# Kernel tuning notes

Hardware: AMD Instinct MI355X
Metric: run time of the kernel (lower is better)

The kernel has to match this reference:

```python
import jax, jax.numpy as jnp
import numpy as np

N = 100000
E = 1000000
IN_C, HID, OUT_C = 64, 64, 40


def setup_inputs() -> dict:
    key = jax.random.key(0)
    ks = jax.random.split(key, 12)
    x = jax.random.normal(ks[0], (N, IN_C), dtype=jnp.float32)
    edge_index = jax.random.randint(ks[1], (2, E), 0, N, dtype=jnp.int64)

    def glorot(k, fan_in, fan_out):
        s = (6.0 / (fan_in + fan_out)) ** 0.5
        return jax.random.uniform(k, (fan_in, fan_out), jnp.float32, -s, s)

    return {
        "x": x,
        "edge_index": edge_index,
        "W1": glorot(ks[2], IN_C, HID), "b1": jnp.zeros((HID,), jnp.float32),
        "W2": glorot(ks[3], HID, HID), "b2": jnp.zeros((HID,), jnp.float32),
        "Wm1": glorot(ks[4], HID, HID), "bm1": jnp.zeros((HID,), jnp.float32),
        "Wm2": glorot(ks[5], HID, OUT_C), "bm2": jnp.zeros((OUT_C,), jnp.float32),
    }


def _gcn_conv(h_in, W, b, src, dst, deg_inv_sqrt):
    # PyG GCNConv: x' = D^{-1/2} (A + I) D^{-1/2} (x W) + b, self-loops added.
    h = h_in @ W                                        # [N, F]
    norm = deg_inv_sqrt[src] * deg_inv_sqrt[dst]        # [E]
    msg = h[src] * norm[:, None]                        # gather + scale
    agg = jax.ops.segment_sum(msg, dst, num_segments=N)  # scatter-add
    # self-loop contribution: deg_i^{-1/2} * deg_i^{-1/2} * h_i
    agg = agg + h * (deg_inv_sqrt * deg_inv_sqrt)[:, None]
    return agg + b


def reference(x, edge_index, W1, b1, W2, b2, Wm1, bm1, Wm2, bm2):
    src, dst = edge_index[0], edge_index[1]
    deg = jax.ops.segment_sum(jnp.ones((E,), jnp.float32), dst, num_segments=N) + 1.0
    deg_inv_sqrt = jax.lax.rsqrt(deg)

    h = _gcn_conv(x, W1, b1, src, dst, deg_inv_sqrt)
    h = jax.nn.relu(h)
    h = _gcn_conv(h, W2, b2, src, dst, deg_inv_sqrt)  # no relu after last conv

    h = jax.nn.relu(h @ Wm1 + bm1)
    out = h @ Wm2 + bm2
    return out
```

## Files before the change

kernel.cpp:

```cpp
#include <hip/hip_runtime.h>
#include <hip/hip_bf16.h>
#include <hip/hip_fp16.h>


namespace {

constexpr int N_NODES = 100000;
constexpr int N_EDGES = 1000000;
constexpr int NBUCK = (N_NODES + 511) / 512;
constexpr int CAP_RAW = 8192;
constexpr int CAP_COL = 12288;
constexpr int EPB_A = 2048;

__global__ __launch_bounds__(256) void bucket_kernel(const void* __restrict__ ei,
                                                     int* __restrict__ bucketCnt,
                                                     unsigned* __restrict__ tmp) {
  __shared__ int hist[NBUCK];
  __shared__ int basePB[NBUCK];
  __shared__ int cur[NBUCK];
  __shared__ int sflag;
  int t = threadIdx.x;
  if (t < NBUCK) { hist[t] = 0; cur[t] = 0; }
  if (t == 0) sflag = 0;
  __syncthreads();

  int e0 = blockIdx.x * EPB_A;
  const unsigned* w = (const unsigned*)ei;
  unsigned any = 0;
#pragma unroll
  for (int s = 0; s < 2; s++) {
    int e = e0 + s * 256 + t;
    if (e < N_EDGES) any |= w[2 * e + 1];
  }
  if (any) sflag = 1;
  __syncthreads();
  int is32 = sflag;

  unsigned wreg[8];
  int breg[8];
#pragma unroll
  for (int k = 0; k < 8; k++) {
    int e = e0 + k * 256 + t;
    breg[k] = -1;
    if (e < N_EDGES) {
      int s, d;
      if (is32) {
        const int* p = (const int*)ei;
        s = p[e]; d = p[N_EDGES + e];
      } else {
        const long long* p = (const long long*)ei;
        s = (int)p[e]; d = (int)p[N_EDGES + e];
      }
      wreg[k] = ((unsigned)s << 9) | (unsigned)(d & 511);
      breg[k] = d >> 9;
      atomicAdd(&hist[breg[k]], 1);
    }
  }
  __syncthreads();
  if (t < NBUCK) basePB[t] = hist[t] ? atomicAdd(&bucketCnt[t], hist[t]) : 0;
  __syncthreads();
#pragma unroll
  for (int k = 0; k < 8; k++) {
    if (breg[k] >= 0) {
      int r = atomicAdd(&cur[breg[k]], 1);
      tmp[(size_t)breg[k] * CAP_RAW + basePB[breg[k]] + r] = wreg[k];
    }
  }
}

__global__ __launch_bounds__(512) void csr_kernel(const unsigned* __restrict__ tmp,
                                                  const int* __restrict__ bucketCnt,
                                                  int* __restrict__ col,
                                                  int* __restrict__ row_start,
                                                  int* __restrict__ row_end,
                                                  float* __restrict__ dinv) {
  __shared__ int sc[512];
  __shared__ int hist[512];
  __shared__ unsigned stage[CAP_RAW];
  int b = blockIdx.x, t = threadIdx.x;
  int myCnt = bucketCnt[b];
  int baseT = b * CAP_RAW;
  int baseC = b * CAP_COL;

  hist[t] = 0;
  __syncthreads();
  for (int i = t; i < myCnt; i += 512) {
    unsigned w = tmp[(size_t)baseT + i];
    stage[i] = w;
    atomicAdd(&hist[w & 511u], 1);
  }
  __syncthreads();

  int deg = hist[t];
  int pdeg = (deg + 15) & ~15;
  sc[t] = pdeg;
  __syncthreads();
#pragma unroll
  for (int off = 1; off < 512; off <<= 1) {
    int u = (t >= off) ? sc[t - off] : 0;
    __syncthreads();
    sc[t] += u;
    __syncthreads();
  }
  int pexcl = sc[t] - pdeg;
  int d = b * 512 + t;
  if (d < N_NODES) {
    row_start[d] = baseC + pexcl;
    row_end[d] = baseC + pexcl + pdeg;
    dinv[d] = rsqrtf((float)deg + 1.0f);
  }
  __syncthreads();
  hist[t] = pexcl;
  __syncthreads();
  for (int i = t; i < myCnt; i += 512) {
    unsigned w = stage[i];
    int pos = atomicAdd(&hist[w & 511u], 1);
    col[baseC + pos] = (int)(w >> 9);
  }
  for (int j = deg; j < pdeg; j++) col[baseC + pexcl + j] = N_NODES;
}

__device__ inline uint4 pack_half8(const float* v) {
  __half2 h0 = __floats2half2_rn(v[0], v[1]);
  __half2 h1 = __floats2half2_rn(v[2], v[3]);
  __half2 h2 = __floats2half2_rn(v[4], v[5]);
  __half2 h3 = __floats2half2_rn(v[6], v[7]);
  uint4 u;
  u.x = *(unsigned*)&h0; u.y = *(unsigned*)&h1;
  u.z = *(unsigned*)&h2; u.w = *(unsigned*)&h3;
  return u;
}

__global__ __launch_bounds__(256) void gemm_g_kernel(const float* __restrict__ A,
                                                     const float* __restrict__ W,
                                                     const float* __restrict__ dinv,
                                                     __half* __restrict__ g,
                                                     __half* __restrict__ gpad2,
                                                     int reluIn) {
  __shared__ float Ws[64 * 64];
  int t = threadIdx.x;
  if (blockIdx.x == 0 && t < 32) {
    ((float*)(g + (size_t)N_NODES * 64))[t] = 0.f;
    if (gpad2) ((float*)(gpad2 + (size_t)N_NODES * 64))[t] = 0.f;
  }
  for (int i = t; i < 64 * 64 / 4; i += 256) ((float4*)Ws)[i] = ((const float4*)W)[i];
  __syncthreads();

  int rg = t >> 3, cg = t & 7;
  int r0 = blockIdx.x * 128 + rg * 4;
  int c0 = cg * 8;

  float acc[4][8];
#pragma unroll
  for (int i = 0; i < 4; i++)
#pragma unroll
    for (int j = 0; j < 8; j++) acc[i][j] = 0.f;

  const float4* A4 = (const float4*)A;
  for (int kk = 0; kk < 16; kk++) {
    float4 a[4];
#pragma unroll
    for (int i = 0; i < 4; i++) {
      int r = r0 + i;
      float4 v = (r < N_NODES) ? A4[(size_t)r * 16 + kk] : make_float4(0.f, 0.f, 0.f, 0.f);
      if (reluIn) {
        v.x = fmaxf(v.x, 0.f); v.y = fmaxf(v.y, 0.f);
        v.z = fmaxf(v.z, 0.f); v.w = fmaxf(v.w, 0.f);
      }
      a[i] = v;
    }
#pragma unroll
    for (int q = 0; q < 4; q++) {
      int k = kk * 4 + q;
      float w[8];
#pragma unroll
      for (int j = 0; j < 2; j++) *(float4*)&w[4 * j] = *(const float4*)&Ws[k * 64 + c0 + 4 * j];
#pragma unroll
      for (int i = 0; i < 4; i++) {
        float av = q == 0 ? a[i].x : q == 1 ? a[i].y : q == 2 ? a[i].z : a[i].w;
#pragma unroll
        for (int j = 0; j < 8; j++) acc[i][j] = fmaf(av, w[j], acc[i][j]);
      }
    }
  }
#pragma unroll
  for (int i = 0; i < 4; i++) {
    int r = r0 + i;
    if (r < N_NODES) {
      float s = dinv[r];
#pragma unroll
      for (int j = 0; j < 8; j++) acc[i][j] *= s;
      *(uint4*)(g + (size_t)r * 64 + c0) = pack_half8(acc[i]);
    }
  }
}

template <int MODE>
__global__ __launch_bounds__(256) void agg_fused(const __half* __restrict__ g,
                                                 const int* __restrict__ col,
                                                 const int* __restrict__ row_start,
                                                 const int* __restrict__ row_end,
                                                 const float* __restrict__ dinv,
                                                 const float* __restrict__ bconv,
                                                 const float* __restrict__ W,
                                                 const float* __restrict__ bpost,
                                                 void* __restrict__ outp) {
  __shared__ float Ws[64 * 64];
  __shared__ float rows[8][64];
  int t = threadIdx.x;
  for (int i = t; i < 64 * 64 / 4; i += 256) ((float4*)Ws)[i] = ((const float4*)W)[i];
  __syncthreads();

  int wave = t >> 6;
  int lane = t & 63;
  int half = lane >> 5;
  int sub = lane & 31;
  int slot = t >> 5;
  int d = blockIdx.x * 8 + wave * 2 + half;

  const __half2* g2 = (const __half2*)g;
  int e0 = row_start[d];
  int len = row_end[d] - e0;

  float2 a0 = __half22float2(g2[(size_t)d * 32 + sub]);
  float2 a1 = {0.f, 0.f}, a2 = {0.f, 0.f}, a3 = {0.f, 0.f};
  float2 a4 = {0.f, 0.f}, a5 = {0.f, 0.f}, a6 = {0.f, 0.f}, a7 = {0.f, 0.f};

  for (int i = 0; i < len; i += 16) {
    int4 ca = *(const int4*)(col + e0 + i);
    int4 cb = *(const int4*)(col + e0 + i + 4);
    int4 cc = *(const int4*)(col + e0 + i + 8);
    int4 cd = *(const int4*)(col + e0 + i + 12);
    float2 h0 = __half22float2(g2[(size_t)ca.x * 32 + sub]);
    float2 h1 = __half22float2(g2[(size_t)ca.y * 32 + sub]);
    float2 h2 = __half22float2(g2[(size_t)ca.z * 32 + sub]);
    float2 h3 = __half22float2(g2[(size_t)ca.w * 32 + sub]);
    float2 h4 = __half22float2(g2[(size_t)cb.x * 32 + sub]);
    float2 h5 = __half22float2(g2[(size_t)cb.y * 32 + sub]);
    float2 h6 = __half22float2(g2[(size_t)cb.z * 32 + sub]);
    float2 h7 = __half22float2(g2[(size_t)cb.w * 32 + sub]);
    float2 h8 = __half22float2(g2[(size_t)cc.x * 32 + sub]);
    float2 h9 = __half22float2(g2[(size_t)cc.y * 32 + sub]);
    float2 hA = __half22float2(g2[(size_t)cc.z * 32 + sub]);
    float2 hB = __half22float2(g2[(size_t)cc.w * 32 + sub]);
    float2 hC = __half22float2(g2[(size_t)cd.x * 32 + sub]);
    float2 hD = __half22float2(g2[(size_t)cd.y * 32 + sub]);
    float2 hE = __half22float2(g2[(size_t)cd.z * 32 + sub]);
    float2 hF = __half22float2(g2[(size_t)cd.w * 32 + sub]);
    a0.x += h0.x; a0.y += h0.y; a1.x += h1.x; a1.y += h1.y;
    a2.x += h2.x; a2.y += h2.y; a3.x += h3.x; a3.y += h3.y;
    a4.x += h4.x; a4.y += h4.y; a5.x += h5.x; a5.y += h5.y;
    a6.x += h6.x; a6.y += h6.y; a7.x += h7.x; a7.y += h7.y;
    a0.x += h8.x; a0.y += h8.y; a1.x += h9.x; a1.y += h9.y;
    a2.x += hA.x; a2.y += hA.y; a3.x += hB.x; a3.y += hB.y;
    a4.x += hC.x; a4.y += hC.y; a5.x += hD.x; a5.y += hD.y;
    a6.x += hE.x; a6.y += hE.y; a7.x += hF.x; a7.y += hF.y;
  }
  float rx = ((a0.x + a1.x) + (a2.x + a3.x)) + ((a4.x + a5.x) + (a6.x + a7.x));
  float ry = ((a0.y + a1.y) + (a2.y + a3.y)) + ((a4.y + a5.y) + (a6.y + a7.y));
  float dv = dinv[d];
  float2 bv = ((const float2*)bconv)[sub];
  float hx = fmaf(rx, dv, bv.x);
  float hy = fmaf(ry, dv, bv.y);
  if (MODE == 1) { hx = fmaxf(hx, 0.f); hy = fmaxf(hy, 0.f); }

  *(float2*)&rows[slot][2 * sub] = make_float2(hx, hy);

  float o0 = 0.f, o1 = 0.f;
#pragma unroll 8
  for (int ks = 0; ks < 32; ks++) {
    float2 hv = *(const float2*)&rows[slot][2 * ks];
    float2 w0 = *(const float2*)&Ws[(2 * ks) * 64 + 2 * sub];
    float2 w1 = *(const float2*)&Ws[(2 * ks + 1) * 64 + 2 * sub];
    o0 = fmaf(hv.x, w0.x, o0);
    o0 = fmaf(hv.y, w1.x, o0);
    o1 = fmaf(hv.x, w0.y, o1);
    o1 = fmaf(hv.y, w1.y, o1);
  }

  if (MODE == 1) {
    o0 *= dv; o1 *= dv;
    __half2 hh = __floats2half2_rn(o0, o1);
    ((__half2*)outp)[(size_t)d * 32 + sub] = hh;
  } else {
    float2 bp = ((const float2*)bpost)[sub];
    float2 o;
    o.x = fmaxf(o0 + bp.x, 0.f);
    o.y = fmaxf(o1 + bp.y, 0.f);
    ((float2*)outp)[(size_t)d * 32 + sub] = o;
  }
}

template <int F>
__global__ __launch_bounds__(256) void gemm_kernel(const float* __restrict__ A, const float* __restrict__ W,
                                                   const float* __restrict__ bias, float* __restrict__ C,
                                                   int n, int reluIn, int reluOut) {
  constexpr int CPT = F / 8;
  __shared__ float Ws[64 * F];
  int t = threadIdx.x;
  for (int i = t; i < 64 * F / 4; i += 256) ((float4*)Ws)[i] = ((const float4*)W)[i];
  __syncthreads();

  int rg = t >> 3, cg = t & 7;
  int r0 = blockIdx.x * 128 + rg * 4;
  int c0 = cg * CPT;

  float acc[4][CPT];
#pragma unroll
  for (int i = 0; i < 4; i++)
#pragma unroll
    for (int j = 0; j < CPT; j++) acc[i][j] = 0.f;

  const float4* A4 = (const float4*)A;
  for (int kk = 0; kk < 16; kk++) {
    float4 a[4];
#pragma unroll
    for (int i = 0; i < 4; i++) {
      int r = r0 + i;
      float4 v = (r < n) ? A4[(size_t)r * 16 + kk] : make_float4(0.f, 0.f, 0.f, 0.f);
      if (reluIn) {
        v.x = fmaxf(v.x, 0.f); v.y = fmaxf(v.y, 0.f);
        v.z = fmaxf(v.z, 0.f); v.w = fmaxf(v.w, 0.f);
      }
      a[i] = v;
    }
#pragma unroll
    for (int q = 0; q < 4; q++) {
      int k = kk * 4 + q;
      float w[CPT];
      if constexpr (CPT % 4 == 0) {
#pragma unroll
        for (int j = 0; j < CPT / 4; j++)
          *(float4*)&w[4 * j] = *(const float4*)&Ws[k * F + c0 + 4 * j];
      } else {
#pragma unroll
        for (int j = 0; j < CPT; j++) w[j] = Ws[k * F + c0 + j];
      }
#pragma unroll
      for (int i = 0; i < 4; i++) {
        float av = q == 0 ? a[i].x : q == 1 ? a[i].y : q == 2 ? a[i].z : a[i].w;
#pragma unroll
        for (int j = 0; j < CPT; j++) acc[i][j] = fmaf(av, w[j], acc[i][j]);
      }
    }
  }

  float bv[CPT];
#pragma unroll
  for (int j = 0; j < CPT; j++) bv[j] = bias ? bias[c0 + j] : 0.f;
#pragma unroll
  for (int i = 0; i < 4; i++) {
    int r = r0 + i;
    if (r < n) {
      float* crow = C + (size_t)r * F + c0;
#pragma unroll
      for (int j = 0; j < CPT; j++) {
        float v = acc[i][j] + bv[j];
        if (reluOut) v = fmaxf(v, 0.f);
        crow[j] = v;
      }
    }
  }
}

}

extern "C" void kernel_launch(void* const* d_in, const int* in_sizes, int n_in,
                              void* d_out, int out_size, void* d_ws, size_t ws_size,
                              hipStream_t stream) {
  const float* x   = (const float*)d_in[0];
  const void*  ei  = d_in[1];
  const float* W1  = (const float*)d_in[2];
  const float* b1  = (const float*)d_in[3];
  const float* W2  = (const float*)d_in[4];
  const float* b2  = (const float*)d_in[5];
  const float* Wm1 = (const float*)d_in[6];
  const float* bm1 = (const float*)d_in[7];
  const float* Wm2 = (const float*)d_in[8];
  const float* bm2 = (const float*)d_in[9];
  float* out = (float*)d_out;

  char* ws = (char*)d_ws;
  size_t off = 0;
  auto alloc = [&](size_t bytes) -> void* {
    void* p = ws + off;
    off = (off + bytes + 511) & ~(size_t)511;
    return p;
  };
  int*      bucketCnt = (int*)     alloc((size_t)NBUCK * 4);
  unsigned* tmp       = (unsigned*)alloc((size_t)NBUCK * CAP_RAW * 4);
  int*      colA      = (int*)     alloc((size_t)NBUCK * CAP_COL * 4);
  int*      rowS      = (int*)     alloc((size_t)N_NODES * 4);
  int*      rowE      = (int*)     alloc((size_t)N_NODES * 4);
  float*    dinv      = (float*)   alloc((size_t)N_NODES * 4);
  __half*   g1        = (__half*)  alloc((size_t)(N_NODES + 1) * 64 * 2);
  __half*   gB        = (__half*)  alloc((size_t)(N_NODES + 1) * 64 * 2);
  float*    hA        = (float*)   alloc((size_t)N_NODES * 64 * 4);
  (void)ws_size; (void)in_sizes; (void)n_in; (void)out_size;

  dim3 b256(256);
  int gGemm = (N_NODES + 127) / 128;
  int gAgg  = N_NODES / 8;
  int gBkt  = (N_EDGES + EPB_A - 1) / EPB_A;

  hipMemsetAsync(bucketCnt, 0, (size_t)NBUCK * 4, stream);
  bucket_kernel<<<gBkt, b256, 0, stream>>>(ei, bucketCnt, tmp);
  csr_kernel<<<NBUCK, dim3(512), 0, stream>>>(tmp, bucketCnt, colA, rowS, rowE, dinv);

  gemm_g_kernel<<<gGemm, b256, 0, stream>>>(x, W1, dinv, g1, gB, 0);

  agg_fused<1><<<gAgg, b256, 0, stream>>>(g1, colA, rowS, rowE, dinv, b1, W2, nullptr, gB);

  agg_fused<2><<<gAgg, b256, 0, stream>>>(gB, colA, rowS, rowE, dinv, b2, Wm1, bm1, hA);

  gemm_kernel<40><<<gGemm, b256, 0, stream>>>(hA, Wm2, bm2, out, N_NODES, 0, 0);
}
```

Before: 249.0 us.

## Fuse final Wm2 projection into second aggregation and shrink CSR buckets

The final 64x40 linear layer is folded into the MODE 2 aggregation kernel using a transposed Wm2 held in shared memory. This drops the fp32 hidden buffer write/read and one kernel launch. The CSR build also switches from 512-node to 128-node buckets with 256-thread blocks, giving more blocks for the bucketing and CSR passes. In exchange, the bucket kernel does more per-block global atomics, and there is less capacity headroom per bucket.

```diff
diff --git a/kernel.cpp b/kernel.cpp
--- a/kernel.cpp
+++ b/kernel.cpp
@@ -7,9 +7,10 @@
 
 constexpr int N_NODES = 100000;
 constexpr int N_EDGES = 1000000;
-constexpr int NBUCK = (N_NODES + 511) / 512;
-constexpr int CAP_RAW = 8192;
-constexpr int CAP_COL = 12288;
+constexpr int BN = 128;
+constexpr int NBUCK = (N_NODES + BN - 1) / BN;
+constexpr int CAP_RAW = 2048;
+constexpr int CAP_COL = 2560;
 constexpr int EPB_A = 2048;
 
 __global__ __launch_bounds__(256) void bucket_kernel(const void* __restrict__ ei,
@@ -20,7 +21,7 @@
   __shared__ int cur[NBUCK];
   __shared__ int sflag;
   int t = threadIdx.x;
-  if (t < NBUCK) { hist[t] = 0; cur[t] = 0; }
+  for (int i = t; i < NBUCK; i += 256) { hist[i] = 0; cur[i] = 0; }
   if (t == 0) sflag = 0;
   __syncthreads();
 
@@ -51,13 +52,14 @@
         const long long* p = (const long long*)ei;
         s = (int)p[e]; d = (int)p[N_EDGES + e];
       }
-      wreg[k] = ((unsigned)s << 9) | (unsigned)(d & 511);
-      breg[k] = d >> 9;
+      wreg[k] = ((unsigned)s << 7) | (unsigned)(d & 127);
+      breg[k] = d >> 7;
       atomicAdd(&hist[breg[k]], 1);
     }
   }
   __syncthreads();
-  if (t < NBUCK) basePB[t] = hist[t] ? atomicAdd(&bucketCnt[t], hist[t]) : 0;
+  for (int i = t; i < NBUCK; i += 256)
+    basePB[i] = hist[i] ? atomicAdd(&bucketCnt[i], hist[i]) : 0;
   __syncthreads();
 #pragma unroll
   for (int k = 0; k < 8; k++) {
@@ -68,56 +70,57 @@
   }
 }
 
-__global__ __launch_bounds__(512) void csr_kernel(const unsigned* __restrict__ tmp,
+__global__ __launch_bounds__(256) void csr_kernel(const unsigned* __restrict__ tmp,
                                                   const int* __restrict__ bucketCnt,
                                                   int* __restrict__ col,
                                                   int* __restrict__ row_start,
                                                   int* __restrict__ row_end,
                                                   float* __restrict__ dinv) {
-  __shared__ int sc[512];
-  __shared__ int hist[512];
+  __shared__ int sc[BN];
+  __shared__ int hist[BN];
   __shared__ unsigned stage[CAP_RAW];
   int b = blockIdx.x, t = threadIdx.x;
   int myCnt = bucketCnt[b];
-  int baseT = b * CAP_RAW;
   int baseC = b * CAP_COL;
-
-  hist[t] = 0;
-  __syncthreads();
-  for (int i = t; i < myCnt; i += 512) {
-    unsigned w = tmp[(size_t)baseT + i];
+  size_t baseT = (size_t)b * CAP_RAW;
+  int nb = min(BN, N_NODES - b * BN);
+
+  if (t < BN) hist[t] = 0;
+  __syncthreads();
+  for (int i = t; i < myCnt; i += 256) {
+    unsigned w = tmp[baseT + i];
     stage[i] = w;
-    atomicAdd(&hist[w & 511u], 1);
-  }
-  __syncthreads();
-
-  int deg = hist[t];
+    atomicAdd(&hist[w & 127u], 1);
+  }
+  __syncthreads();
+
+  int deg = (t < BN) ? hist[t] : 0;
   int pdeg = (deg + 15) & ~15;
-  sc[t] = pdeg;
-  __syncthreads();
-#pragma unroll
-  for (int off = 1; off < 512; off <<= 1) {
-    int u = (t >= off) ? sc[t - off] : 0;
+  if (t < BN) sc[t] = pdeg;
+  __syncthreads();
+  for (int off = 1; off < BN; off <<= 1) {
+    int u = (t >= off && t < BN) ? sc[t - off] : 0;
     __syncthreads();
-    sc[t] += u;
+    if (t < BN) sc[t] += u;
     __syncthreads();
   }
-  int pexcl = sc[t] - pdeg;
-  int d = b * 512 + t;
-  if (d < N_NODES) {
+  int pexcl = (t < BN) ? sc[t] - pdeg : 0;
+  int d = b * BN + t;
+  if (t < nb) {
     row_start[d] = baseC + pexcl;
     row_end[d] = baseC + pexcl + pdeg;
     dinv[d] = rsqrtf((float)deg + 1.0f);
   }
   __syncthreads();
-  hist[t] = pexcl;
-  __syncthreads();
-  for (int i = t; i < myCnt; i += 512) {
+  if (t < BN) hist[t] = pexcl;
+  __syncthreads();
+  for (int i = t; i < myCnt; i += 256) {
     unsigned w = stage[i];
-    int pos = atomicAdd(&hist[w & 511u], 1);
-    col[baseC + pos] = (int)(w >> 9);
-  }
-  for (int j = deg; j < pdeg; j++) col[baseC + pexcl + j] = N_NODES;
+    int pos = atomicAdd(&hist[w & 127u], 1);
+    col[baseC + pos] = (int)(w >> 7);
+  }
+  if (t < nb)
+    for (int j = deg; j < pdeg; j++) col[baseC + pexcl + j] = N_NODES;
 }
 
 __device__ inline uint4 pack_half8(const float* v) {
@@ -204,11 +207,20 @@
                                                  const float* __restrict__ bconv,
                                                  const float* __restrict__ W,
                                                  const float* __restrict__ bpost,
+                                                 const float* __restrict__ Wm2,
+                                                 const float* __restrict__ bm2,
                                                  void* __restrict__ outp) {
   __shared__ float Ws[64 * 64];
   __shared__ float rows[8][64];
+  __shared__ float Wm2t[(MODE == 2) ? 40 : 1][65];
   int t = threadIdx.x;
   for (int i = t; i < 64 * 64 / 4; i += 256) ((float4*)Ws)[i] = ((const float4*)W)[i];
+  if (MODE == 2) {
+    for (int i = t; i < 64 * 40; i += 256) {
+      int k = i / 40, c = i % 40;
+      Wm2t[c][k] = Wm2[i];
+    }
+  }
   __syncthreads();
 
   int wave = t >> 6;
@@ -284,82 +296,27 @@
     ((__half2*)outp)[(size_t)d * 32 + sub] = hh;
   } else {
     float2 bp = ((const float2*)bpost)[sub];
-    float2 o;
-    o.x = fmaxf(o0 + bp.x, 0.f);
-    o.y = fmaxf(o1 + bp.y, 0.f);
-    ((float2*)outp)[(size_t)d * 32 + sub] = o;
-  }
-}
-
-template <int F>
-__global__ __launch_bounds__(256) void gemm_kernel(const float* __restrict__ A, const float* __restrict__ W,
-                                                   const float* __restrict__ bias, float* __restrict__ C,
-                                                   int n, int reluIn, int reluOut) {
-  constexpr int CPT = F / 8;
-  __shared__ float Ws[64 * F];
-  int t = threadIdx.x;
-  for (int i = t; i < 64 * F / 4; i += 256) ((float4*)Ws)[i] = ((const float4*)W)[i];
-  __syncthreads();
-
-  int rg = t >> 3, cg = t & 7;
-  int r0 = blockIdx.x * 128 + rg * 4;
-  int c0 = cg * CPT;
-
-  float acc[4][CPT];
-#pragma unroll
-  for (int i = 0; i < 4; i++)
-#pragma unroll
-    for (int j = 0; j < CPT; j++) acc[i][j] = 0.f;
-
-  const float4* A4 = (const float4*)A;
-  for (int kk = 0; kk < 16; kk++) {
-    float4 a[4];
-#pragma unroll
-    for (int i = 0; i < 4; i++) {
-      int r = r0 + i;
-      float4 v = (r < n) ? A4[(size_t)r * 16 + kk] : make_float4(0.f, 0.f, 0.f, 0.f);
-      if (reluIn) {
-        v.x = fmaxf(v.x, 0.f); v.y = fmaxf(v.y, 0.f);
-        v.z = fmaxf(v.z, 0.f); v.w = fmaxf(v.w, 0.f);
+    float h3a = fmaxf(o0 + bp.x, 0.f);
+    float h3b = fmaxf(o1 + bp.y, 0.f);
+    *(float2*)&rows[slot][2 * sub] = make_float2(h3a, h3b);
+
+    float p0 = 0.f, p1 = 0.f;
+    int c1 = sub + 32;
+#pragma unroll 4
+    for (int k4 = 0; k4 < 64; k4 += 4) {
+      float4 hv = *(const float4*)&rows[slot][k4];
+      float4 wa = *(const float4*)&Wm2t[sub][k4];
+      p0 = fmaf(hv.x, wa.x, p0); p0 = fmaf(hv.y, wa.y, p0);
+      p0 = fmaf(hv.z, wa.z, p0); p0 = fmaf(hv.w, wa.w, p0);
+      if (sub < 8) {
+        float4 wb = *(const float4*)&Wm2t[c1][k4];
+        p1 = fmaf(hv.x, wb.x, p1); p1 = fmaf(hv.y, wb.y, p1);
+        p1 = fmaf(hv.z, wb.z, p1); p1 = fmaf(hv.w, wb.w, p1);
       }
-      a[i] = v;
-    }
-#pragma unroll
-    for (int q = 0; q < 4; q++) {
-      int k = kk * 4 + q;
-      float w[CPT];
-      if constexpr (CPT % 4 == 0) {
-#pragma unroll
-        for (int j = 0; j < CPT / 4; j++)
-          *(float4*)&w[4 * j] = *(const float4*)&Ws[k * F + c0 + 4 * j];
-      } else {
-#pragma unroll
-        for (int j = 0; j < CPT; j++) w[j] = Ws[k * F + c0 + j];
-      }
-#pragma unroll
-      for (int i = 0; i < 4; i++) {
-        float av = q == 0 ? a[i].x : q == 1 ? a[i].y : q == 2 ? a[i].z : a[i].w;
-#pragma unroll
-        for (int j = 0; j < CPT; j++) acc[i][j] = fmaf(av, w[j], acc[i][j]);
-      }
-    }
-  }
-
-  float bv[CPT];
-#pragma unroll
-  for (int j = 0; j < CPT; j++) bv[j] = bias ? bias[c0 + j] : 0.f;
-#pragma unroll
-  for (int i = 0; i < 4; i++) {
-    int r = r0 + i;
-    if (r < n) {
-      float* crow = C + (size_t)r * F + c0;
-#pragma unroll
-      for (int j = 0; j < CPT; j++) {
-        float v = acc[i][j] + bv[j];
-        if (reluOut) v = fmaxf(v, 0.f);
-        crow[j] = v;
-      }
-    }
+    }
+    float* op = (float*)outp;
+    op[(size_t)d * 40 + sub] = p0 + bm2[sub];
+    if (sub < 8) op[(size_t)d * 40 + c1] = p1 + bm2[c1];
   }
 }
 
@@ -395,7 +352,6 @@
   float*    dinv      = (float*)   alloc((size_t)N_NODES * 4);
   __half*   g1        = (__half*)  alloc((size_t)(N_NODES + 1) * 64 * 2);
   __half*   gB        = (__half*)  alloc((size_t)(N_NODES + 1) * 64 * 2);
-  float*    hA        = (float*)   alloc((size_t)N_NODES * 64 * 4);
   (void)ws_size; (void)in_sizes; (void)n_in; (void)out_size;
 
   dim3 b256(256);
@@ -405,13 +361,13 @@
 
   hipMemsetAsync(bucketCnt, 0, (size_t)NBUCK * 4, stream);
   bucket_kernel<<<gBkt, b256, 0, stream>>>(ei, bucketCnt, tmp);
-  csr_kernel<<<NBUCK, dim3(512), 0, stream>>>(tmp, bucketCnt, colA, rowS, rowE, dinv);
+  csr_kernel<<<NBUCK, b256, 0, stream>>>(tmp, bucketCnt, colA, rowS, rowE, dinv);
 
   gemm_g_kernel<<<gGemm, b256, 0, stream>>>(x, W1, dinv, g1, gB, 0);
 
-  agg_fused<1><<<gAgg, b256, 0, stream>>>(g1, colA, rowS, rowE, dinv, b1, W2, nullptr, gB);
-
-  agg_fused<2><<<gAgg, b256, 0, stream>>>(gB, colA, rowS, rowE, dinv, b2, Wm1, bm1, hA);
-
-  gemm_kernel<40><<<gGemm, b256, 0, stream>>>(hA, Wm2, bm2, out, N_NODES, 0, 0);
-}
+  agg_fused<1><<<gAgg, b256, 0, stream>>>(g1, colA, rowS, rowE, dinv, b1, W2,
+                                          nullptr, nullptr, nullptr, gB);
+
+  agg_fused<2><<<gAgg, b256, 0, stream>>>(gB, colA, rowS, rowE, dinv, b2, Wm1,
+                                          bm1, Wm2, bm2, out);
+}
```

Result: slower. 276.5 us (+11.1%).
